# Kernel optimization log

Hardware: AMD Instinct MI355X
Metric: run time of the kernel (lower is better)

The kernel has to match this reference:

```python
import jax, jax.numpy as jnp
import numpy as np

B, S, D, L, E, C = 4, 512, 768, 10, 25, 9  # batch, seq, enc dim, max span len, len-embed dim, n labels


def _span_ids(seq_len, max_span_len):
    # replicates get_all_span_ids: distinct (start, min(start+k, seq_len)) for k in 1..max_span_len
    starts, ends = [], []
    for i in range(seq_len):
        seen = set()
        for k in range(1, max_span_len + 1):
            e = min(i + k, seq_len)
            if e not in seen:
                seen.add(e)
                starts.append(i)
                ends.append(e)
    return np.asarray(starts, np.int32), np.asarray(ends, np.int32)


def setup_inputs() -> dict:
    key = jax.random.key(0)
    k1, k2, k3 = jax.random.split(key, 3)
    st, en = _span_ids(S, L)  # N = 5075 spans
    return {
        "word_encodings": jax.random.normal(k1, (B, S, D), jnp.float32),
        "len_embed": jax.random.normal(k2, (L, E), jnp.float32) * 0.02,
        "W": jax.random.normal(k3, (D + E, C), jnp.float32) * 0.02,
        "b": jnp.zeros((C,), jnp.float32),
        "span_starts": jnp.asarray(st),
        "span_ends": jnp.asarray(en),
    }


def reference(word_encodings, len_embed, W, b, span_starts, span_ends):
    # word_encodings: [B,S,D]; span_starts/ends: [N] with end - start <= L
    N = span_starts.shape[0]
    pos = span_starts[:, None] + jnp.arange(L, dtype=span_starts.dtype)  # [N,L]
    valid = pos < span_ends[:, None]                                     # [N,L]
    pos_c = jnp.minimum(pos, S - 1)
    gathered = word_encodings[:, pos_c]                                  # [B,N,L,D]
    neg = jnp.asarray(-1e30, word_encodings.dtype)
    pooled = jnp.max(jnp.where(valid[None, :, :, None], gathered, neg), axis=2)  # [B,N,D]
    lens = span_ends - span_starts - 1                                   # [N] in [0, L)
    le = jnp.broadcast_to(len_embed[lens][None], (pooled.shape[0], N, E))  # [B,N,E]
    rep = jnp.concatenate([pooled, le], axis=-1)                         # [B,N,D+E]
    scores = jnp.einsum('bnf,fc->bnc', rep, W) + b                       # [B,N,C]
    return scores
```

## Files before the change

### kernel.cpp

```cpp
#include <hip/hip_runtime.h>


#define SS 512
#define DD 768
#define LL 10
#define EE 25
#define CC 9
#define NSPANS 5075
#define BB 4

__global__ __launch_bounds__(256) void spanner_kernel(
    const float* __restrict__ we,
    const float* __restrict__ lene,
    const float* __restrict__ W,
    const float* __restrict__ bias,
    float* __restrict__ out)
{
    __shared__ float lenW[LL][CC];
    const int t = threadIdx.x;

    if (t < LL * CC) {
        const int l = t / CC, c = t % CC;
        float s = bias[c];
#pragma unroll
        for (int e = 0; e < EE; ++e)
            s += lene[l * EE + e] * W[(DD + e) * CC + c];
        lenW[l][c] = s;
    }
    __syncthreads();

    const int lane = t & 63;
    const int gid  = blockIdx.x * 4 + (t >> 6);
    const int b    = gid >> 9;
    const int i    = gid & (SS - 1);
    const int cnt  = min(LL, SS - i);
    const int base = (i <= SS - LL + 1) ? i * LL
                     : (NSPANS - ((SS - i) * (SS + 1 - i)) / 2);

    float Wr[3][4][CC];
#pragma unroll
    for (int c0 = 0; c0 < 3; ++c0)
#pragma unroll
        for (int q = 0; q < 4; ++q) {
            const int d = c0 * 256 + lane * 4 + q;
#pragma unroll
            for (int c = 0; c < CC; ++c)
                Wr[c0][q][c] = W[d * CC + c];
        }

    const float4* rowbase = reinterpret_cast<const float4*>(we) + (size_t)(b * SS) * (DD / 4);

    float4 r0, r1, r2;
    {
        const float4* rp = rowbase + (size_t)i * (DD / 4);
        r0 = rp[lane]; r1 = rp[64 + lane]; r2 = rp[128 + lane];
    }

    float m[3][4];
#pragma unroll
    for (int c0 = 0; c0 < 3; ++c0)
#pragma unroll
        for (int q = 0; q < 4; ++q) m[c0][q] = -INFINITY;

    float* const outb = out + ((size_t)b * NSPANS + base) * CC;

#pragma unroll
    for (int k = 0; k < LL; ++k) {
        if (k >= cnt) break;

        {
            const float* f;
            f = (const float*)&r0;
#pragma unroll
            for (int q = 0; q < 4; ++q) m[0][q] = fmaxf(m[0][q], f[q]);
            f = (const float*)&r1;
#pragma unroll
            for (int q = 0; q < 4; ++q) m[1][q] = fmaxf(m[1][q], f[q]);
            f = (const float*)&r2;
#pragma unroll
            for (int q = 0; q < 4; ++q) m[2][q] = fmaxf(m[2][q], f[q]);
        }

        if (k + 1 < cnt) {
            const float4* rp = rowbase + (size_t)(i + k + 1) * (DD / 4);
            r0 = rp[lane]; r1 = rp[64 + lane]; r2 = rp[128 + lane];
        }

        float acc[CC];
#pragma unroll
        for (int c = 0; c < CC; ++c) acc[c] = 0.0f;
#pragma unroll
        for (int c0 = 0; c0 < 3; ++c0)
#pragma unroll
            for (int q = 0; q < 4; ++q)
#pragma unroll
                for (int c = 0; c < CC; ++c)
                    acc[c] = fmaf(m[c0][q], Wr[c0][q][c], acc[c]);

#pragma unroll
        for (int mask = 1; mask < 64; mask <<= 1)
#pragma unroll
            for (int c = 0; c < CC; ++c)
                acc[c] += __shfl_xor(acc[c], mask, 64);

        float v = acc[0];
        v = (lane == 1) ? acc[1] : v;
        v = (lane == 2) ? acc[2] : v;
        v = (lane == 3) ? acc[3] : v;
        v = (lane == 4) ? acc[4] : v;
        v = (lane == 5) ? acc[5] : v;
        v = (lane == 6) ? acc[6] : v;
        v = (lane == 7) ? acc[7] : v;
        v = (lane == 8) ? acc[8] : v;
        if (lane < CC)
            outb[(size_t)k * CC + lane] = v + lenW[k][lane];
    }
}

extern "C" void kernel_launch(void* const* d_in, const int* in_sizes, int n_in,
                              void* d_out, int out_size, void* d_ws, size_t ws_size,
                              hipStream_t stream) {
    const float* we   = (const float*)d_in[0];
    const float* lene = (const float*)d_in[1];
    const float* W    = (const float*)d_in[2];
    const float* bias = (const float*)d_in[3];
    float* out        = (float*)d_out;

    spanner_kernel<<<512, 256, 0, stream>>>(we, lene, W, bias, out);
}
```

Measured before the change: 85.32 us.

## Use DPP wave reductions, batch span reductions, and vectorize weight loads

```diff
diff --git a/kernel.cpp b/kernel.cpp
--- a/kernel.cpp
+++ b/kernel.cpp
@@ -7,9 +7,23 @@
 #define EE 25
 #define CC 9
 #define NSPANS 5075
-#define BB 4
 
-__global__ __launch_bounds__(256) void spanner_kernel(
+__device__ __forceinline__ float wave_sum64(float v) {
+    int x;
+    x = __builtin_amdgcn_update_dpp(0, __float_as_int(v), 0xB1, 0xF, 0xF, true);
+    v += __int_as_float(x);
+    x = __builtin_amdgcn_update_dpp(0, __float_as_int(v), 0x4E, 0xF, 0xF, true);
+    v += __int_as_float(x);
+    x = __builtin_amdgcn_update_dpp(0, __float_as_int(v), 0x141, 0xF, 0xF, true);
+    v += __int_as_float(x);
+    x = __builtin_amdgcn_update_dpp(0, __float_as_int(v), 0x140, 0xF, 0xF, true);
+    v += __int_as_float(x);
+    v += __shfl_xor(v, 16, 64);
+    v += __shfl_xor(v, 32, 64);
+    return v;
+}
+
+__global__ __launch_bounds__(256, 2) void spanner_kernel(
     const float* __restrict__ we,
     const float* __restrict__ lene,
     const float* __restrict__ W,
@@ -34,27 +48,29 @@
     const int b    = gid >> 9;
     const int i    = gid & (SS - 1);
     const int cnt  = min(LL, SS - i);
-    const int base = (i <= SS - LL + 1) ? i * LL
-                     : (NSPANS - ((SS - i) * (SS + 1 - i)) / 2);
+    const int base = (i <= SS - LL) ? i * LL
+                     : (NSPANS - ((SS - i) * (SS - i + 1)) / 2);
 
     float Wr[3][4][CC];
 #pragma unroll
-    for (int c0 = 0; c0 < 3; ++c0)
+    for (int c0 = 0; c0 < 3; ++c0) {
+        const float4* wp = reinterpret_cast<const float4*>(W + (c0 * 256 + lane * 4) * CC);
+        float4 wv[9];
 #pragma unroll
-        for (int q = 0; q < 4; ++q) {
-            const int d = c0 * 256 + lane * 4 + q;
+        for (int j = 0; j < 9; ++j) wv[j] = wp[j];
+        const float* wf = reinterpret_cast<const float*>(wv);
+#pragma unroll
+        for (int q = 0; q < 4; ++q)
 #pragma unroll
             for (int c = 0; c < CC; ++c)
-                Wr[c0][q][c] = W[d * CC + c];
-        }
+                Wr[c0][q][c] = wf[q * CC + c];
+    }
 
     const float4* rowbase = reinterpret_cast<const float4*>(we) + (size_t)(b * SS) * (DD / 4);
 
-    float4 r0, r1, r2;
-    {
-        const float4* rp = rowbase + (size_t)i * (DD / 4);
-        r0 = rp[lane]; r1 = rp[64 + lane]; r2 = rp[128 + lane];
-    }
+    float4 r0 = rowbase[(size_t)i * (DD / 4) + lane];
+    float4 r1 = rowbase[(size_t)i * (DD / 4) + 64 + lane];
+    float4 r2 = rowbase[(size_t)i * (DD / 4) + 128 + lane];
 
     float m[3][4];
 #pragma unroll
@@ -62,12 +78,11 @@
 #pragma unroll
         for (int q = 0; q < 4; ++q) m[c0][q] = -INFINITY;
 
-    float* const outb = out + ((size_t)b * NSPANS + base) * CC;
+    float acc[5][CC];
+    float res[LL];
 
 #pragma unroll
     for (int k = 0; k < LL; ++k) {
-        if (k >= cnt) break;
-
         {
             const float* f;
             f = (const float*)&r0;
@@ -81,39 +96,43 @@
             for (int q = 0; q < 4; ++q) m[2][q] = fmaxf(m[2][q], f[q]);
         }
 
-        if (k + 1 < cnt) {
-            const float4* rp = rowbase + (size_t)(i + k + 1) * (DD / 4);
-            r0 = rp[lane]; r1 = rp[64 + lane]; r2 = rp[128 + lane];
+        if (k + 1 < LL) {
+            const int nr = min(i + k + 1, SS - 1);
+            r0 = rowbase[(size_t)nr * (DD / 4) + lane];
+            r1 = rowbase[(size_t)nr * (DD / 4) + 64 + lane];
+            r2 = rowbase[(size_t)nr * (DD / 4) + 128 + lane];
         }
 
-        float acc[CC];
+        const int kk = k % 5;
 #pragma unroll
-        for (int c = 0; c < CC; ++c) acc[c] = 0.0f;
+        for (int c = 0; c < CC; ++c) acc[kk][c] = 0.0f;
 #pragma unroll
         for (int c0 = 0; c0 < 3; ++c0)
 #pragma unroll
             for (int q = 0; q < 4; ++q)
 #pragma unroll
                 for (int c = 0; c < CC; ++c)
-                    acc[c] = fmaf(m[c0][q], Wr[c0][q][c], acc[c]);
+                    acc[kk][c] = fmaf(m[c0][q], Wr[c0][q][c], acc[kk][c]);
 
+        if (kk == 4) {
 #pragma unroll
-        for (int mask = 1; mask < 64; mask <<= 1)
+            for (int kb = 0; kb < 5; ++kb) {
+                float s[CC];
 #pragma unroll
-            for (int c = 0; c < CC; ++c)
-                acc[c] += __shfl_xor(acc[c], mask, 64);
+                for (int c = 0; c < CC; ++c) s[c] = wave_sum64(acc[kb][c]);
+                float v = s[0];
+#pragma unroll
+                for (int c = 1; c < CC; ++c) v = (lane == c) ? s[c] : v;
+                res[k - 4 + kb] = v;
+            }
+        }
+    }
 
-        float v = acc[0];
-        v = (lane == 1) ? acc[1] : v;
-        v = (lane == 2) ? acc[2] : v;
-        v = (lane == 3) ? acc[3] : v;
-        v = (lane == 4) ? acc[4] : v;
-        v = (lane == 5) ? acc[5] : v;
-        v = (lane == 6) ? acc[6] : v;
-        v = (lane == 7) ? acc[7] : v;
-        v = (lane == 8) ? acc[8] : v;
-        if (lane < CC)
-            outb[(size_t)k * CC + lane] = v + lenW[k][lane];
+    float* const outb = out + ((size_t)b * NSPANS + base) * CC;
+    if (lane < CC) {
+#pragma unroll
+        for (int k = 0; k < LL; ++k)
+            if (k < cnt) outb[k * CC + lane] = res[k] + lenW[k][lane];
     }
 }
 
```

After: 79.56 us. -6.7%, faster.
